# Optimization experiments

Hardware: AMD Instinct MI355X
Metric: run time of the kernel (lower is better)

Reference implementation:

```python
import jax, jax.numpy as jnp
import numpy as np

MAX_SEQ = 4096
HEADS = 4
LOCAL_HEADS = 1
WINDOW = 128
B, N, D_IN, D, D_OUT = 8, 3000, 128, 512, 64


def setup_inputs():
    key = jax.random.key(0)
    ks = jax.random.split(key, 9)
    s = 0.02
    return {
        'x': jax.random.normal(ks[0], (B, N, D_IN), jnp.float32),
        'W1': jax.random.normal(ks[1], (D_IN, D), jnp.float32) * s,
        'b1': jnp.zeros((D,), jnp.float32),
        'ln1_g': jnp.ones((D,), jnp.float32),
        'ln1_b': jnp.zeros((D,), jnp.float32),
        'Wq': jax.random.normal(ks[2], (D, D), jnp.float32) * s,
        'Wk': jax.random.normal(ks[3], (D, D), jnp.float32) * s,
        'Wv': jax.random.normal(ks[4], (D, D), jnp.float32) * s,
        'Wo': jax.random.normal(ks[5], (D, D), jnp.float32) * s,
        'bo': jnp.zeros((D,), jnp.float32),
        'ln2_g': jnp.ones((D,), jnp.float32),
        'ln2_b': jnp.zeros((D,), jnp.float32),
        'Wf1': jax.random.normal(ks[6], (D, 4 * D), jnp.float32) * s,
        'bf1': jnp.zeros((4 * D,), jnp.float32),
        'Wf2': jax.random.normal(ks[7], (4 * D, D), jnp.float32) * s,
        'bf2': jnp.zeros((D,), jnp.float32),
        'W2': jax.random.normal(ks[8], (D, D_OUT), jnp.float32) * s,
        'b2': jnp.zeros((D_OUT,), jnp.float32),
    }


def _ln(x, g, b, eps=1e-5):
    mu = jnp.mean(x, -1, keepdims=True)
    var = jnp.var(x, -1, keepdims=True)
    return (x - mu) * jax.lax.rsqrt(var + eps) * g + b


def _look_around(x, pad_value=0.0):
    # x: [b, w, n, ...] -> [b, w, 3n, ...] (backward=1, self, forward=1 windows)
    pads = [(0, 0), (1, 1)] + [(0, 0)] * (x.ndim - 2)
    p = jnp.pad(x, pads, constant_values=pad_value)
    w = x.shape[1]
    return jnp.concatenate([p[:, i:i + w] for i in range(3)], axis=2)


def _local_attn(q, k, v):
    # windowed softmax attention, window=128, look back/forward 1 window
    Bh, H, T, d = q.shape
    w = T // WINDOW
    merge = lambda t: t.reshape(Bh * H, w, WINDOW, d)
    bq, bk, bv = merge(q), merge(k), merge(v)
    bk = _look_around(bk)
    bv = _look_around(bv)
    ticker = jnp.arange(T).reshape(1, w, WINDOW)
    bq_k = _look_around(ticker, pad_value=-1)  # [1, w, 3*WINDOW]
    dots = jnp.einsum('bwie,bwje->bwij', bq, bk) * (d ** -0.5)
    mask = (bq_k[:, :, None, :] == -1)
    dots = jnp.where(mask, jnp.finfo(dots.dtype).min, dots)
    attn = jax.nn.softmax(dots, axis=-1)
    out = jnp.einsum('bwij,bwje->bwie', attn, bv)
    return out.reshape(Bh, H, T, d)


def _linear_attn(q, k, v):
    # kernelized global attention: softmax feature maps + d x d context
    d = q.shape[-1]
    q = jax.nn.softmax(q, axis=-1) * (d ** -0.5)
    k = jax.nn.softmax(k, axis=-2)
    ctx = jnp.einsum('bhnd,bhne->bhde', k, v)
    return jnp.einsum('bhnd,bhde->bhne', q, ctx)


def _self_attn(x, Wq, Wk, Wv, Wo, bo):
    Bx, T, Dm = x.shape
    dh = Dm // HEADS
    split = lambda t: t.reshape(Bx, T, HEADS, dh).transpose(0, 2, 1, 3)
    q, k, v = split(x @ Wq), split(x @ Wk), split(x @ Wv)
    lq, gq = q[:, :LOCAL_HEADS], q[:, LOCAL_HEADS:]
    lk, gk = k[:, :LOCAL_HEADS], k[:, LOCAL_HEADS:]
    lv, gv = v[:, :LOCAL_HEADS], v[:, LOCAL_HEADS:]
    local_out = _local_attn(lq, lk, lv)
    global_out = _linear_attn(gq, gk, gv)
    out = jnp.concatenate([local_out, global_out], axis=1)
    out = out.transpose(0, 2, 1, 3).reshape(Bx, T, Dm)
    return out @ Wo + bo


def _forward(x, W1, b1, ln1_g, ln1_b, Wq, Wk, Wv, Wo, bo,
             ln2_g, ln2_b, Wf1, bf1, Wf2, bf2, W2, b2):
    Bx, n, _ = x.shape
    xp = jnp.pad(x, ((0, 0), (0, MAX_SEQ - n), (0, 0)))
    h = jnp.tanh(xp @ W1 + b1)
    # depth=1 transformer block: PreNorm attn + residual, PreNorm FF + residual
    h = h + _self_attn(_ln(h, ln1_g, ln1_b), Wq, Wk, Wv, Wo, bo)
    ff = jax.nn.gelu(_ln(h, ln2_g, ln2_b) @ Wf1 + bf1, approximate=False)
    h = h + ff @ Wf2 + bf2
    out = h @ W2 + b2
    return out[:, :n, :]


def reference(x, W1, b1, ln1_g, ln1_b, Wq, Wk, Wv, Wo, bo,
              ln2_g, ln2_b, Wf1, bf1, Wf2, bf2, W2, b2):
    return _forward(x, W1, b1, ln1_g, ln1_b, Wq, Wk, Wv, Wo, bo,
                    ln2_g, ln2_b, Wf1, bf1, Wf2, bf2, W2, b2)
```

## Files before the change

### kernel.cpp

```cpp
#include <hip/hip_runtime.h>
#include <hip/hip_bf16.h>
#include <math.h>


typedef __hip_bfloat16 bf16;
typedef __attribute__((ext_vector_type(8))) short short8;
typedef __attribute__((ext_vector_type(4))) float floatx4;

#define SEQ   4096
#define NBAT  8
#define DM    512
#define DINP  128
#define DFF   2048
#define NREAL 3000
#define CS    40

#define MFMA16(a,b,c) __builtin_amdgcn_mfma_f32_16x16x32_bf16((a),(b),(c),0,0,0)
#define BARRIER() asm volatile("s_barrier" ::: "memory")

__device__ __forceinline__ void gload_lds16(const void* g, void* l) {
  auto* gp = reinterpret_cast<const __attribute__((address_space(1))) unsigned int*>(
      reinterpret_cast<uintptr_t>(g));
  auto* lp = reinterpret_cast<__attribute__((address_space(3))) unsigned int*>(
      reinterpret_cast<uintptr_t>(l));
  __builtin_amdgcn_global_load_lds(gp, lp, 16, 0, 0);
}

__device__ __forceinline__ short8 lds_read128(const bf16* p) {
  auto* lp = reinterpret_cast<const __attribute__((address_space(3))) bf16*>(
      reinterpret_cast<uintptr_t>(p));
  short8 r;
  asm volatile("ds_read_b128 %0, %1" : "=v"(r) : "v"(lp));
  return r;
}

__device__ __forceinline__ float fast_erff(float x) {
  float ax = fabsf(x);
  float t = __builtin_amdgcn_rcpf(fmaf(0.3275911f, ax, 1.f));
  float p = fmaf(fmaf(fmaf(fmaf(1.061405429f, t, -1.453152027f), t,
                           1.421413741f), t, -0.284496736f), t, 0.254829592f) * t;
  float r = 1.f - p * __expf(-ax * ax);
  return copysignf(r, x);
}

__device__ __forceinline__ float fast_tanhf(float x) {
  float e = __expf(2.f * x);
  return 1.f - 2.f * __builtin_amdgcn_rcpf(e + 1.f);
}

__global__ __launch_bounds__(256) void beacon(float* __restrict__ out, long n) {
  long i = (long)blockIdx.x * 256 + threadIdx.x;
  if (i < n) out[i] = 10000.f;
}

__global__ __launch_bounds__(256) void transpose8(
    const float* __restrict__ W1, const float* __restrict__ Wq,
    const float* __restrict__ Wk, const float* __restrict__ Wv,
    const float* __restrict__ Wo, const float* __restrict__ Wf1,
    const float* __restrict__ Wf2, const float* __restrict__ W2,
    bf16* __restrict__ wt) {
  const int Ks[8]   = {128, 512, 512, 512, 512, 512, 2048, 512};
  const int Ns[8]   = {512, 512, 512, 512, 512, 2048, 512, 64};
  const int Nps[8]  = {512, 512, 512, 512, 512, 2048, 512, 128};
  const long Ofs[8] = {0L, 65536L, 327680L, 589824L, 851968L, 1114112L, 2162688L, 3211264L};
  int zi = blockIdx.z;
  int K = Ks[zi], N = Ns[zi], Npad = Nps[zi];
  int k0 = blockIdx.x * 64, n0 = blockIdx.y * 64;
  if (k0 >= K || n0 >= Npad) return;
  const float* W = zi == 0 ? W1 : zi == 1 ? Wq : zi == 2 ? Wk : zi == 3 ? Wv
                 : zi == 4 ? Wo : zi == 5 ? Wf1 : zi == 6 ? Wf2 : W2;
  bf16* Wt = wt + Ofs[zi];
  __shared__ float t[64][65];
  int r = threadIdx.x >> 2, c = (threadIdx.x & 3) * 16;
#pragma unroll
  for (int i = 0; i < 16; i++) {
    int n = n0 + c + i;
    t[r][c + i] = (n < N) ? W[(long)(k0 + r) * N + n] : 0.f;
  }
  __syncthreads();
#pragma unroll
  for (int i = 0; i < 16; i++)
    Wt[(long)(n0 + r) * K + k0 + c + i] = (bf16)t[c + i][r];
}

__device__ inline uint4 pack8(const float* p) {
  union { bf16 h[8]; uint4 u; } r;
  float4 a = *(const float4*)p;
  float4 b = *(const float4*)(p + 4);
  r.h[0] = (bf16)a.x; r.h[1] = (bf16)a.y; r.h[2] = (bf16)a.z; r.h[3] = (bf16)a.w;
  r.h[4] = (bf16)b.x; r.h[5] = (bf16)b.y; r.h[6] = (bf16)b.z; r.h[7] = (bf16)b.w;
  return r.u;
}

__global__ __launch_bounds__(512, 2) void gemm256(
    const bf16* __restrict__ A, const bf16* __restrict__ Bt,
    const float* __restrict__ bias, float* __restrict__ Cf, bf16* __restrict__ Cb,
    int K, int lda, int ldb, int ldc, int EPI,
    long aBatch, long bBatch, int zdiv, long cOuter, long cInner) {
  __shared__ __align__(16) bf16 sm[5 * 256 * 64];
  bf16* const smB = sm + 2 * 16384;
  const int tid = threadIdx.x;
  const int lane = tid & 63, wid = tid >> 6;

  const int nx = gridDim.x, ny = gridDim.y;
  const long nwg = (long)nx * ny * gridDim.z;
  const long fid = blockIdx.x + (long)nx * (blockIdx.y + (long)ny * blockIdx.z);
  const long cq = nwg >> 3, cr = nwg & 7;
  const long xcd = fid & 7, ofs = fid >> 3;
  const long swz = (xcd < cr ? xcd * (cq + 1) : cr * (cq + 1) + (xcd - cr) * cq) + ofs;
  const int bx = (int)(swz % nx);
  const int by = (int)((swz / nx) % ny);
  const int bz = (int)(swz / ((long)nx * ny));

  const bf16* Ab = A + (long)bz * aBatch;
  const bf16* Bb = Bt + (long)bz * bBatch;
  const long cOff = (long)(bz / zdiv) * cOuter + (long)(bz % zdiv) * cInner;
  const int row0 = by * 256;
  const int col0 = bx * 256;

  const int widm = wid >> 2, widn = wid & 3;
  const int lr = lane & 15, lq4 = lane >> 4;
  const int sw = (lr & 7) << 4;
  const int k0e = ((0 * 64 + lq4 * 16) ^ sw) >> 1;
  const int k1e = ((1 * 64 + lq4 * 16) ^ sw) >> 1;

  const int lrow = lane >> 3;
  const int lch = (lane & 7) ^ lrow;
  const bf16* pAbase = Ab + (long)(row0 + wid * 8 + lrow) * lda + lch * 8;
  const bf16* pBbase = Bb + (long)(col0 + wid * 8 + lrow) * ldb + lch * 8;
  const long a64 = (long)64 * lda, b64 = (long)64 * ldb;
  int kA = 0, kB = 0;

  floatx4 acc[8][4];
#pragma unroll
  for (int i = 0; i < 8; i++)
#pragma unroll
    for (int j = 0; j < 4; j++) acc[i][j] = {0.f, 0.f, 0.f, 0.f};

  auto stageA4 = [&](int buf) {
    bf16* base = sm + buf * 16384;
#pragma unroll
    for (int h = 0; h < 2; h++) {
      bf16* d = base + (h * 128 + wid * 8) * 64;
      const bf16* g = pAbase + (long)(h * 2) * a64 + kA;
      gload_lds16(g, d);
      gload_lds16(g + a64, d + 64 * 64);
    }
    kA += 64;
  };
  auto stageB4 = [&](int slot) {
    bf16* base = smB + slot * 16384;
#pragma unroll
    for (int h = 0; h < 2; h++) {
      bf16* d = base + (h * 128 + wid * 8) * 64;
      const bf16* g = pBbase + (long)(h * 2) * b64 + kB;
      gload_lds16(g, d);
      gload_lds16(g + b64, d + 64 * 64);
    }
    kB += 64;
  };

  short8 bfr[4][2], af[2][2];
  auto readB = [&](int slot) {
    const bf16* base = smB + slot * 16384;
#pragma unroll
    for (int nt = 0; nt < 4; nt++) {
      int colB = widn * 64 + nt * 16 + lr;
      bfr[nt][0] = lds_read128(base + colB * 64 + k0e);
      bfr[nt][1] = lds_read128(base + colB * 64 + k1e);
    }
  };
  auto readA = [&](int buf, int q) {
    const bf16* base = sm + buf * 16384;
#pragma unroll
    for (int m = 0; m < 2; m++) {
      int rowA = widm * 128 + q * 32 + m * 16 + lr;
      af[m][0] = lds_read128(base + rowA * 64 + k0e);
      af[m][1] = lds_read128(base + rowA * 64 + k1e);
    }
  };
  auto mmaq = [&](int q) {
    asm volatile("s_waitcnt lgkmcnt(0)" ::: "memory");
    __builtin_amdgcn_sched_barrier(0);
    __builtin_amdgcn_s_setprio(1);
#pragma unroll
    for (int m = 0; m < 2; m++)
#pragma unroll
      for (int nt = 0; nt < 4; nt++) {
        acc[q * 2 + m][nt] = MFMA16(af[m][0], bfr[nt][0], acc[q * 2 + m][nt]);
        acc[q * 2 + m][nt] = MFMA16(af[m][1], bfr[nt][1], acc[q * 2 + m][nt]);
      }
    __builtin_amdgcn_s_setprio(0);
  };

  const int T = K >> 6;
  stageA4(0);
  stageB4(0);
  stageB4(1);
  asm volatile("s_waitcnt vmcnt(4)" ::: "memory");
  BARRIER();

  int bsel = 0;
  for (int t = 0; t < T; t++) {
    const int cb = t & 1, nb = cb ^ 1;
    readB(bsel);
    readA(cb, 0);
    if (t + 1 < T) stageA4(nb);
    mmaq(0);
    readA(cb, 1);
    mmaq(1);
    readA(cb, 2);
    if (t + 2 < T) stageB4(bsel == 0 ? 2 : bsel - 1);
    mmaq(2);
    readA(cb, 3);
    mmaq(3);
    if (t + 2 < T) {
      asm volatile("s_waitcnt vmcnt(4)" ::: "memory");
    } else if (t + 1 < T) {
      asm volatile("s_waitcnt vmcnt(0)" ::: "memory");
    }
    BARRIER();
    bsel = bsel == 2 ? 0 : bsel + 1;
  }

  if (EPI == 2) {
#pragma unroll
    for (int nt = 0; nt < 4; nt++) {
      int c = col0 + widn * 64 + nt * 16 + lr;
      float bv = bias ? bias[c] : 0.f;
#pragma unroll
      for (int mi = 0; mi < 8; mi++) {
        long rb = row0 + widm * 128 + mi * 16 + lq4 * 4;
#pragma unroll
        for (int reg = 0; reg < 4; reg++) {
          float v = acc[mi][nt][reg] + bv;
          long idx = cOff + (rb + reg) * (long)ldc + c;
          Cf[idx] += v;
        }
      }
    }
  } else {
    bf16* scr = sm + wid * (64 * 72);
    const int rr = lane >> 3, ccol = (lane & 7) * 8;
#pragma unroll
    for (int p = 0; p < 2; p++) {
#pragma unroll
      for (int nt = 0; nt < 4; nt++) {
        int c = col0 + widn * 64 + nt * 16 + lr;
        float bv = bias ? bias[c] : 0.f;
#pragma unroll
        for (int ml = 0; ml < 4; ml++) {
#pragma unroll
          for (int reg = 0; reg < 4; reg++) {
            float v = acc[p * 4 + ml][nt][reg] + bv;
            if (EPI == 4) v = 0.5f * v * (1.f + fast_erff(v * 0.70710678118654752f));
            scr[(ml * 16 + lq4 * 4 + reg) * 72 + nt * 16 + lr] = (bf16)v;
          }
        }
      }
#pragma unroll
      for (int it = 0; it < 8; it++) {
        int r = it * 8 + rr;
        uint4 v = *(const uint4*)&scr[r * 72 + ccol];
        long grow = row0 + widm * 128 + p * 64 + r;
        *(uint4*)&Cb[cOff + grow * (long)ldc + col0 + widn * 64 + ccol] = v;
      }
    }
  }
}

__global__ __launch_bounds__(256) void gemm_bt(
    const void* __restrict__ Avoid, const bf16* __restrict__ Bt,
    const float* __restrict__ bias, float* __restrict__ Cf, bf16* __restrict__ Cb,
    int K, int lda, int ldb, int ldc, int EPI, int AMODE,
    long aBatch, long bBatch, int zdiv, long cOuter, long cInner) {
  __shared__ __align__(16) bf16 As0[128 * 32];
  __shared__ __align__(16) bf16 As1[128 * 32];
  __shared__ __align__(16) bf16 Bs0[128 * 32];
  __shared__ __align__(16) bf16 Bs1[128 * 32];
  const int tid = threadIdx.x;

  const int nx = gridDim.x, ny = gridDim.y;
  const long nwg = (long)nx * ny * gridDim.z;
  const long fid = blockIdx.x + (long)nx * (blockIdx.y + (long)ny * blockIdx.z);
  const long cq = nwg >> 3, cr = nwg & 7;
  const long xcd = fid & 7, ofs = fid >> 3;
  const long swz = (xcd < cr ? xcd * (cq + 1) : cr * (cq + 1) + (xcd - cr) * cq) + ofs;
  const int bx = (int)(swz % nx);
  const int by = (int)((swz / nx) % ny);
  const int bz = (int)(swz / ((long)nx * ny));

  Bt += (long)bz * bBatch;
  const long cOff = (long)(bz / zdiv) * cOuter + (long)(bz % zdiv) * cInner;
  const int row0 = by * 128;
  const int col0 = bx * 128;
  const int lane = tid & 63, wid = tid >> 6;
  const int wm = (wid & 1) * 64, wn = (wid >> 1) * 64;
  const int lr = lane & 15, lk = (lane >> 4) * 8;

  floatx4 acc[4][4];
#pragma unroll
  for (int i = 0; i < 4; i++)
#pragma unroll
    for (int j = 0; j < 4; j++) acc[i][j] = {0.f, 0.f, 0.f, 0.f};

  if (AMODE == 0) {
    const bf16* A = (const bf16*)Avoid + (long)bz * aBatch;
    const bf16* pAa = A + (long)(row0 + wid * 16 + (lane >> 2)) * lda + (lane & 3) * 8;
    const bf16* pBa = Bt + (long)(col0 + wid * 16 + (lane >> 2)) * ldb + (lane & 3) * 8;
    bf16* ldsA0 = &As0[wid * 16 * 32];
    bf16* ldsA1 = &As1[wid * 16 * 32];
    bf16* ldsB0 = &Bs0[wid * 16 * 32];
    bf16* ldsB1 = &Bs1[wid * 16 * 32];
    const long a64 = (long)64 * lda, b64 = (long)64 * ldb;

    auto stage = [&](bf16* dA, bf16* dB) {
      gload_lds16(pAa, dA);
      gload_lds16(pAa + a64, dA + 64 * 32);
      gload_lds16(pBa, dB);
      gload_lds16(pBa + b64, dB + 64 * 32);
      pAa += 32; pBa += 32;
    };
    auto compute = [&](const bf16* AS, const bf16* BS) {
      short8 af[4], bfr[4];
#pragma unroll
      for (int mt = 0; mt < 4; mt++) af[mt] = *(const short8*)(&AS[(wm + mt * 16 + lr) * 32 + lk]);
#pragma unroll
      for (int nt = 0; nt < 4; nt++) bfr[nt] = *(const short8*)(&BS[(wn + nt * 16 + lr) * 32 + lk]);
#pragma unroll
      for (int mt = 0; mt < 4; mt++)
#pragma unroll
        for (int nt = 0; nt < 4; nt++)
          acc[mt][nt] = MFMA16(af[mt], bfr[nt], acc[mt][nt]);
    };

    stage(ldsA0, ldsB0);
    __syncthreads();
    for (int k0 = 0; k0 < K; k0 += 64) {
      stage(ldsA1, ldsB1);
      compute(As0, Bs0);
      __syncthreads();
      if (k0 + 64 < K) stage(ldsA0, ldsB0);
      compute(As1, Bs1);
      __syncthreads();
    }
  } else {
    const float* Af = (const float*)Avoid;
    const int srow = tid >> 2;
    const int skcol = (tid & 3) * 8;
    const long r0 = row0 + srow, r1 = r0 + 64;
    const bf16* pB = Bt + (long)(col0 + srow) * ldb + skcol;
    const int ldsOff = srow * 32 + skcol;
    const float* pF0; const float* pF1;
    bool v0 = true, v1 = true;
    if (AMODE == 1) {
      int t0 = (int)(r0 & (SEQ - 1)), t1 = (int)(r1 & (SEQ - 1));
      v0 = t0 < NREAL; v1 = t1 < NREAL;
      if (!v0) t0 = 0;
      if (!v1) t1 = 0;
      pF0 = Af + ((r0 >> 12) * NREAL + t0) * DINP + skcol;
      pF1 = Af + ((r1 >> 12) * NREAL + t1) * DINP + skcol;
    } else {
      pF0 = Af + r0 * lda + skcol;
      pF1 = Af + r1 * lda + skcol;
    }
    for (int k0 = 0; k0 < K; k0 += 32) {
      uint4 b0 = *(const uint4*)(pB);
      uint4 b1 = *(const uint4*)(pB + (long)64 * ldb);
      pB += 32;
      uint4 a0 = {0, 0, 0, 0}, a1 = {0, 0, 0, 0};
      if (v0) a0 = pack8(pF0);
      if (v1) a1 = pack8(pF1);
      pF0 += 32; pF1 += 32;
      __syncthreads();
      *(uint4*)(&As0[ldsOff]) = a0;
      *(uint4*)(&As0[ldsOff + 64 * 32]) = a1;
      *(uint4*)(&Bs0[ldsOff]) = b0;
      *(uint4*)(&Bs0[ldsOff + 64 * 32]) = b1;
      __syncthreads();
      short8 af[4], bfr[4];
#pragma unroll
      for (int mt = 0; mt < 4; mt++) af[mt] = *(const short8*)(&As0[(wm + mt * 16 + lr) * 32 + lk]);
#pragma unroll
      for (int nt = 0; nt < 4; nt++) bfr[nt] = *(const short8*)(&Bs0[(wn + nt * 16 + lr) * 32 + lk]);
#pragma unroll
      for (int mt = 0; mt < 4; mt++)
#pragma unroll
        for (int nt = 0; nt < 4; nt++)
          acc[mt][nt] = MFMA16(af[mt], bfr[nt], acc[mt][nt]);
    }
  }

#pragma unroll
  for (int nt = 0; nt < 4; nt++) {
    int c = col0 + wn + nt * 16 + lr;
    float bv = 0.f;
    if (bias) {
      if (EPI == 5) { if (c < 64) bv = bias[c]; }
      else bv = bias[c];
    }
#pragma unroll
    for (int mt = 0; mt < 4; mt++) {
      long rb = row0 + wm + mt * 16 + (lane >> 4) * 4;
#pragma unroll
      for (int reg = 0; reg < 4; reg++) {
        float v = acc[mt][nt][reg] + bv;
        long ri = rb + reg;
        long idx = cOff + ri * (long)ldc + c;
        if (EPI == 0) Cf[idx] = fast_tanhf(v);
        else if (EPI == 1) Cb[idx] = (bf16)v;
        else if (EPI == 2) Cf[idx] += v;
        else if (EPI == 4) { float g = 0.5f * v * (1.f + fast_erff(v * 0.70710678118654752f)); Cb[idx] = (bf16)g; }
        else if (EPI == 5) {
          int bb = (int)(ri >> 12); int tt = (int)(ri & (SEQ - 1));
          if (tt < NREAL && c < 64) Cf[((long)bb * NREAL + tt) * 64 + c] = v;
        }
      }
    }
  }
}

__global__ __launch_bounds__(256) void ln_kernel(const float* __restrict__ h,
                                                 const float* __restrict__ g,
                                                 const float* __restrict__ bta,
                                                 bf16* __restrict__ out) {
  int wid = threadIdx.x >> 6, lane = threadIdx.x & 63;
  long row = (long)blockIdx.x * 4 + wid;
  const float* src = h + row * DM + lane * 8;
  float4 a = *(const float4*)(src);
  float4 b = *(const float4*)(src + 4);
  float x[8] = {a.x, a.y, a.z, a.w, b.x, b.y, b.z, b.w};
  float s = 0.f, sq = 0.f;
#pragma unroll
  for (int i = 0; i < 8; i++) { s += x[i]; sq += x[i] * x[i]; }
#pragma unroll
  for (int m = 32; m >= 1; m >>= 1) { s += __shfl_xor(s, m, 64); sq += __shfl_xor(sq, m, 64); }
  float mu = s * (1.f / DM);
  float var = sq * (1.f / DM) - mu * mu;
  float rstd = rsqrtf(var + 1e-5f);
  const float* gp = g + lane * 8;
  const float* bp = bta + lane * 8;
  bf16* dst = out + row * DM + lane * 8;
#pragma unroll
  for (int i = 0; i < 8; i++)
    dst[i] = (bf16)((x[i] - mu) * rstd * gp[i] + bp[i]);
}

__global__ __launch_bounds__(256) void local_attn(const bf16* __restrict__ q,
                                                  const bf16* __restrict__ k,
                                                  const bf16* __restrict__ v,
                                                  bf16* __restrict__ att) {
  int half = blockIdx.x, w = blockIdx.y, b = blockIdx.z;
  int tid = threadIdx.x, wid = tid >> 6, lane = tid & 63;
  int lr = lane & 15, lq4 = lane >> 4;
  __shared__ __align__(16) bf16 Ks[32 * 128];
  __shared__ __align__(16) bf16 Vts[128 * 32];
  __shared__ __align__(16) bf16 Ps[4][16 * 32];

  int t0 = w * 128 + half * 64 + wid * 16;
  long qbase = ((long)b * SEQ + t0 + lr) * DM;
  short8 qf[4];
#pragma unroll
  for (int ks = 0; ks < 4; ks++) qf[ks] = *(const short8*)(q + qbase + ks * 32 + lq4 * 8);

  floatx4 Oacc[8];
#pragma unroll
  for (int i = 0; i < 8; i++) Oacc[i] = {0.f, 0.f, 0.f, 0.f};
  float rs[4] = {0.f, 0.f, 0.f, 0.f};

  int keystart = w * 128 - 128;
  for (int ch = 0; ch < 12; ch++) {
    int kb = keystart + ch * 32;
    if (kb < 0 || kb >= SEQ) continue;
    {
      int j = tid >> 3, d = (tid & 7) * 16;
      const bf16* ksrc = k + ((long)b * SEQ + kb + j) * DM + d;
      *(uint4*)(&Ks[j * 128 + d]) = *(const uint4*)(ksrc);
      *(uint4*)(&Ks[j * 128 + d + 8]) = *(const uint4*)(ksrc + 8);
      const bf16* vsrc = v + ((long)b * SEQ + kb + j) * DM + d;
#pragma unroll
      for (int e = 0; e < 16; e++) Vts[(d + e) * 32 + j] = vsrc[e];
    }
    __syncthreads();
    floatx4 s0 = {0.f, 0.f, 0.f, 0.f}, s1 = {0.f, 0.f, 0.f, 0.f};
#pragma unroll
    for (int ks = 0; ks < 4; ks++) {
      short8 kf0 = *(const short8*)(&Ks[(0 + lr) * 128 + ks * 32 + lq4 * 8]);
      short8 kf1 = *(const short8*)(&Ks[(16 + lr) * 128 + ks * 32 + lq4 * 8]);
      s0 = MFMA16(qf[ks], kf0, s0);
      s1 = MFMA16(qf[ks], kf1, s1);
    }
#pragma unroll
    for (int reg = 0; reg < 4; reg++) {
      float e0 = __expf(s0[reg] * 0.08838834764831845f);
      float e1 = __expf(s1[reg] * 0.08838834764831845f);
      rs[reg] += e0 + e1;
      Ps[wid][(lq4 * 4 + reg) * 32 + lr] = (bf16)e0;
      Ps[wid][(lq4 * 4 + reg) * 32 + 16 + lr] = (bf16)e1;
    }
    __syncthreads();
    short8 pf = *(const short8*)(&Ps[wid][lr * 32 + lq4 * 8]);
#pragma unroll
    for (int nt = 0; nt < 8; nt++) {
      short8 vf = *(const short8*)(&Vts[(nt * 16 + lr) * 32 + lq4 * 8]);
      Oacc[nt] = MFMA16(pf, vf, Oacc[nt]);
    }
    __syncthreads();
  }
#pragma unroll
  for (int m = 1; m < 16; m <<= 1)
#pragma unroll
    for (int reg = 0; reg < 4; reg++) rs[reg] += __shfl_xor(rs[reg], m, 64);
  long obase = ((long)b * SEQ + t0 + lq4 * 4) * DM;
#pragma unroll
  for (int nt = 0; nt < 8; nt++)
#pragma unroll
    for (int reg = 0; reg < 4; reg++)
      att[obase + (long)reg * DM + nt * 16 + lr] = (bf16)(Oacc[nt][reg] / rs[reg]);
}

__global__ __launch_bounds__(256) void qp_softmax(const bf16* __restrict__ q, bf16* __restrict__ qp) {
  int wid = threadIdx.x >> 6, lane = threadIdx.x & 63;
  long task = (long)blockIdx.x * 4 + wid;
  int tt = (int)(task & (SEQ - 1));
  int z6 = (int)(task >> 12);
  int lb = z6 / 3, h2 = z6 % 3;
  const bf16* src = q + ((long)lb * SEQ + tt) * DM + (h2 + 1) * 128 + lane * 2;
  float x0 = (float)src[0], x1 = (float)src[1];
  float m = fmaxf(x0, x1);
#pragma unroll
  for (int s = 32; s >= 1; s >>= 1) m = fmaxf(m, __shfl_xor(m, s, 64));
  float e0 = __expf(x0 - m), e1 = __expf(x1 - m);
  float sm = e0 + e1;
#pragma unroll
  for (int s = 32; s >= 1; s >>= 1) sm += __shfl_xor(sm, s, 64);
  float inv = 0.08838834764831845f / sm;
  bf16* dst = qp + task * 128 + lane * 2;
  dst[0] = (bf16)(e0 * inv);
  dst[1] = (bf16)(e1 * inv);
}

__global__ __launch_bounds__(128) void kstats_part(const bf16* __restrict__ k,
                                                   float* __restrict__ part, int lOff) {
  int chunk = blockIdx.x, z = blockIdx.y;
  int lb = z / 3, h2 = z % 3, ch = (h2 + 1) * 128;
  int d = threadIdx.x;
  const bf16* base = k + ((long)lb * SEQ + chunk * 128) * DM + ch + d;
  float m = -1e30f;
#pragma unroll 4
  for (int t = 0; t < 128; t++) m = fmaxf(m, (float)base[(long)t * DM]);
  float l = 0.f;
#pragma unroll 4
  for (int t = 0; t < 128; t++) l += __expf((float)base[(long)t * DM] - m);
  int idx = (z * 32 + chunk) * 128 + d;
  part[idx] = m;
  part[lOff + idx] = l;
}

__global__ __launch_bounds__(128) void kstats_comb(const float* __restrict__ part,
                                                   float* __restrict__ kml, int lOff) {
  int z = blockIdx.x, d = threadIdx.x;
  float M = -1e30f;
#pragma unroll 4
  for (int c = 0; c < 32; c++) M = fmaxf(M, part[(z * 32 + c) * 128 + d]);
  float L = 0.f;
#pragma unroll 4
  for (int c = 0; c < 32; c++) {
    int i = (z * 32 + c) * 128 + d;
    L += part[lOff + i] * __expf(part[i] - M);
  }
  kml[z * 256 + d] = M;
  kml[z * 256 + 128 + d] = L;
}

__global__ __launch_bounds__(256) void ctx_mfma(const bf16* __restrict__ k,
                                                const bf16* __restrict__ v,
                                                const float* __restrict__ kml,
                                                float* __restrict__ part) {
  int chunk = blockIdx.x, z = blockIdx.y;
  int lb = z / 3, h2 = z % 3, ch = (h2 + 1) * 128;
  int tid = threadIdx.x, lane = tid & 63, wid = tid >> 6;
  const int wm = (wid & 1) * 64, wn = (wid >> 1) * 64;
  const int lr = lane & 15, lk = (lane >> 4) * 8;
  __shared__ float ml2[128];
  __shared__ __align__(16) bf16 Vt[128 * CS];
  __shared__ __align__(16) bf16 Kt[128 * CS];
  if (tid < 128)
    ml2[tid] = kml[z * 256 + tid] + logf(kml[z * 256 + 128 + tid]);

  int j = tid >> 3, d0 = (tid & 7) * 16;
  const bf16* vsrc = v + ((long)lb * SEQ + chunk * 512 + j) * DM + ch + d0;
  const bf16* ksrc = k + ((long)lb * SEQ + chunk * 512 + j) * DM + ch + d0;

  floatx4 acc[4][4];
#pragma unroll
  for (int i = 0; i < 4; i++)
#pragma unroll
    for (int jj = 0; jj < 4; jj++) acc[i][jj] = {0.f, 0.f, 0.f, 0.f};

  for (int s = 0; s < 16; s++) {
    union { bf16 h[16]; uint4 u[2]; } va, ka;
    va.u[0] = *(const uint4*)(vsrc); va.u[1] = *(const uint4*)(vsrc + 8);
    ka.u[0] = *(const uint4*)(ksrc); ka.u[1] = *(const uint4*)(ksrc + 8);
    vsrc += (long)32 * DM; ksrc += (long)32 * DM;
    __syncthreads();
#pragma unroll
    for (int e = 0; e < 16; e++) {
      Vt[(d0 + e) * CS + j] = va.h[e];
      Kt[(d0 + e) * CS + j] = (bf16)__expf((float)ka.h[e] - ml2[d0 + e]);
    }
    __syncthreads();
    short8 af[4], bfr[4];
#pragma unroll
    for (int mt = 0; mt < 4; mt++) af[mt] = *(const short8*)(&Vt[(wm + mt * 16 + lr) * CS + lk]);
#pragma unroll
    for (int nt = 0; nt < 4; nt++) bfr[nt] = *(const short8*)(&Kt[(wn + nt * 16 + lr) * CS + lk]);
#pragma unroll
    for (int mt = 0; mt < 4; mt++)
#pragma unroll
      for (int nt = 0; nt < 4; nt++)
        acc[mt][nt] = MFMA16(af[mt], bfr[nt], acc[mt][nt]);
  }

  float* dst = part + ((long)z * 8 + chunk) * 16384;
#pragma unroll
  for (int nt = 0; nt < 4; nt++) {
    int c = wn + nt * 16 + lr;
#pragma unroll
    for (int mt = 0; mt < 4; mt++) {
      int rb = wm + mt * 16 + (lane >> 4) * 4;
#pragma unroll
      for (int reg = 0; reg < 4; reg++)
        dst[(rb + reg) * 128 + c] = acc[mt][nt][reg];
    }
  }
}

__global__ __launch_bounds__(256) void ctx_reduce(const float* __restrict__ part, bf16* __restrict__ ctxT) {
  long i = (long)blockIdx.x * 256 + threadIdx.x;
  int z = (int)(i >> 14);
  int off = (int)(i & 16383);
  float s = 0.f;
#pragma unroll
  for (int c = 0; c < 8; c++) s += part[(((long)z * 8 + c) << 14) + off];
  ctxT[i] = (bf16)s;
}

extern "C" void kernel_launch(void* const* d_in, const int* in_sizes, int n_in,
                              void* d_out, int out_size, void* d_ws, size_t ws_size,
                              hipStream_t stream) {
  float* outp = (float*)d_out;

  long offH = 0;
  int GB = 0;
  long offLNG, offQ, offK, offV, offATT, offCTXP, offCTXT, offKML, offWT, need;
  for (int gb = 8; gb >= 2; gb >>= 1) {
    long sLN = (long)gb * 4194304;
    offLNG = 67108864L;
    offQ   = offLNG + sLN;
    offK   = offQ + sLN;
    offV   = offK + sLN;
    offATT = offV + sLN;
    offCTXP= offATT + sLN;
    offCTXT= offCTXP + (long)gb * 1572864;
    offKML = offCTXT + (long)gb * 98304;
    offWT  = offKML + (long)gb * 3072;
    need   = offWT + 6553600L;
    if ((size_t)need <= ws_size) { GB = gb; break; }
  }
  if (GB == 0) {
    beacon<<<(out_size + 255) / 256, 256, 0, stream>>>(outp, out_size);
    return;
  }
  const int NG = NBAT / GB;
  const long GR = (long)GB * SEQ;
  const int NZ = GB * 3;

  const float* x   = (const float*)d_in[0];
  const float* W1  = (const float*)d_in[1];
  const float* b1  = (const float*)d_in[2];
  const float* g1  = (const float*)d_in[3];
  const float* be1 = (const float*)d_in[4];
  const float* Wq  = (const float*)d_in[5];
  const float* Wk  = (const float*)d_in[6];
  const float* Wv  = (const float*)d_in[7];
  const float* Wo  = (const float*)d_in[8];
  const float* bo  = (const float*)d_in[9];
  const float* g2  = (const float*)d_in[10];
  const float* be2 = (const float*)d_in[11];
  const float* Wf1 = (const float*)d_in[12];
  const float* bf1 = (const float*)d_in[13];
  const float* Wf2 = (const float*)d_in[14];
  const float* bf2 = (const float*)d_in[15];
  const float* W2  = (const float*)d_in[16];
  const float* b2  = (const float*)d_in[17];

  char* ws = (char*)d_ws;
  float* h   = (float*)(ws + offH);
  bf16* lnG  = (bf16*)(ws + offLNG);
  bf16* qp   = (bf16*)(ws + offLNG);
  bf16* qb   = (bf16*)(ws + offQ);
  bf16* kb   = (bf16*)(ws + offK);
  bf16* vb   = (bf16*)(ws + offV);
  bf16* attb = (bf16*)(ws + offATT);
  bf16* ff1g = (bf16*)(ws + offQ);
  float* ctxp= (float*)(ws + offCTXP);
  bf16* ctxT = (bf16*)(ws + offCTXT);
  float* kml = (float*)(ws + offKML);
  bf16* wt   = (bf16*)(ws + offWT);
  bf16* wqt  = wt + 65536;
  bf16* wot  = wt + 851968;
  bf16* wf1t = wt + 1114112;
  bf16* wf2t = wt + 2162688;
  bf16* w2t  = wt + 3211264;
  const int lOff = NZ * 32 * 128;

  transpose8<<<dim3(32, 32, 8), 256, 0, stream>>>(W1, Wq, Wk, Wv, Wo, Wf1, Wf2, W2, wt);

  gemm_bt<<<dim3(4, 256, 1), 256, 0, stream>>>(x, wt, b1, h, nullptr,
      DINP, DINP, DINP, DM, 0, 1, 0, 0, 1, 0, 0);

  for (int g = 0; g < NG; g++) {
    float* hg = h + (long)g * GR * DM;
    ln_kernel<<<(int)(GR / 4), 256, 0, stream>>>(hg, g1, be1, lnG);
    gemm256<<<dim3(2, (int)(GR / 256), 3), 512, 0, stream>>>(lnG, wqt, nullptr, nullptr, qb,
        DM, DM, DM, DM, 1,
        0L, 262144L, 3, 0L, GR * DM);

    local_attn<<<dim3(2, 32, GB), 256, 0, stream>>>(qb, kb, vb, attb);

    qp_softmax<<<NZ * 1024, 256, 0, stream>>>(qb, qp);
    kstats_part<<<dim3(32, NZ), 128, 0, stream>>>(kb, ctxp, lOff);
    kstats_comb<<<NZ, 128, 0, stream>>>(ctxp, kml, lOff);
    ctx_mfma<<<dim3(8, NZ), 256, 0, stream>>>(kb, vb, kml, ctxp);
    ctx_reduce<<<NZ * 64, 256, 0, stream>>>(ctxp, ctxT);
    gemm_bt<<<dim3(1, 32, NZ), 256, 0, stream>>>(qp, ctxT, nullptr, nullptr, attb + 128,
        128, 128, 128, DM, 1, 0,
        (long)SEQ * 128, 16384L, 3, (long)SEQ * DM, 128L);

    gemm256<<<dim3(2, (int)(GR / 256), 1), 512, 0, stream>>>(attb, wot, bo, hg, nullptr,
        DM, DM, DM, DM, 2, 0, 0, 1, 0, 0);
  }

  for (int g = 0; g < NG; g++) {
    float* hg = h + (long)g * GR * DM;
    ln_kernel<<<(int)(GR / 4), 256, 0, stream>>>(hg, g2, be2, lnG);
    gemm256<<<dim3(8, (int)(GR / 256), 1), 512, 0, stream>>>(lnG, wf1t, bf1, nullptr, ff1g,
        DM, DM, DM, DFF, 4, 0, 0, 1, 0, 0);
    gemm256<<<dim3(2, (int)(GR / 256), 1), 512, 0, stream>>>(ff1g, wf2t, bf2, hg, nullptr,
        DFF, DFF, DFF, DM, 2, 0, 0, 1, 0, 0);
  }

  gemm_bt<<<dim3(1, 256, 1), 256, 0, stream>>>(h, w2t, b2, outp, nullptr,
      DM, DM, DM, 64, 5, 2, 0, 0, 1, 0, 0);
}
```

Before: 650.2 us.

## Store residual stream in fp16 and vectorize residual-add epilogue through LDS

The fp32 residual buffer h becomes fp16 throughout: the first GEMM writes tanh output as half, layernorm reads half, the output GEMM packs half to bf16, and the gemm256 residual-add epilogue stages results in LDS and does vectorized 16-byte read-modify-write in half. It also reorders the block-index decomposition so the z index varies fastest after the XCD swizzle. This halves residual-stream traffic and replaces scattered scalar fp32 += with coalesced vector updates, at the cost of fp16 precision and range in the residual accumulation.

```diff
diff --git a/kernel.cpp b/kernel.cpp
--- a/kernel.cpp
+++ b/kernel.cpp
@@ -1,5 +1,6 @@
 #include <hip/hip_runtime.h>
 #include <hip/hip_bf16.h>
+#include <hip/hip_fp16.h>
 #include <math.h>
 
 
@@ -92,9 +93,18 @@
   return r.u;
 }
 
+__device__ inline uint4 pack8h(const __half* p) {
+  union { __half h[8]; uint4 u; } s;
+  s.u = *(const uint4*)p;
+  union { bf16 h[8]; uint4 u; } r;
+#pragma unroll
+  for (int i = 0; i < 8; i++) r.h[i] = (bf16)(float)s.h[i];
+  return r.u;
+}
+
 __global__ __launch_bounds__(512, 2) void gemm256(
     const bf16* __restrict__ A, const bf16* __restrict__ Bt,
-    const float* __restrict__ bias, float* __restrict__ Cf, bf16* __restrict__ Cb,
+    const float* __restrict__ bias, __half* __restrict__ Ch, bf16* __restrict__ Cb,
     int K, int lda, int ldb, int ldc, int EPI,
     long aBatch, long bBatch, int zdiv, long cOuter, long cInner) {
   __shared__ __align__(16) bf16 sm[5 * 256 * 64];
@@ -102,15 +112,16 @@
   const int tid = threadIdx.x;
   const int lane = tid & 63, wid = tid >> 6;
 
-  const int nx = gridDim.x, ny = gridDim.y;
-  const long nwg = (long)nx * ny * gridDim.z;
+  const int nx = gridDim.x, ny = gridDim.y, nz = gridDim.z;
+  const long nwg = (long)nx * ny * nz;
   const long fid = blockIdx.x + (long)nx * (blockIdx.y + (long)ny * blockIdx.z);
   const long cq = nwg >> 3, cr = nwg & 7;
   const long xcd = fid & 7, ofs = fid >> 3;
   const long swz = (xcd < cr ? xcd * (cq + 1) : cr * (cq + 1) + (xcd - cr) * cq) + ofs;
-  const int bx = (int)(swz % nx);
-  const int by = (int)((swz / nx) % ny);
-  const int bz = (int)(swz / ((long)nx * ny));
+  const int bz = (int)(swz % nz);
+  const long s2 = swz / nz;
+  const int bx = (int)(s2 % nx);
+  const int by = (int)(s2 / nx);
 
   const bf16* Ab = A + (long)bz * aBatch;
   const bf16* Bb = Bt + (long)bz * bBatch;
@@ -224,19 +235,34 @@
   }
 
   if (EPI == 2) {
-#pragma unroll
-    for (int nt = 0; nt < 4; nt++) {
-      int c = col0 + widn * 64 + nt * 16 + lr;
-      float bv = bias ? bias[c] : 0.f;
-#pragma unroll
-      for (int mi = 0; mi < 8; mi++) {
-        long rb = row0 + widm * 128 + mi * 16 + lq4 * 4;
-#pragma unroll
-        for (int reg = 0; reg < 4; reg++) {
-          float v = acc[mi][nt][reg] + bv;
-          long idx = cOff + (rb + reg) * (long)ldc + c;
-          Cf[idx] += v;
+    __half* scr = (__half*)sm + wid * (64 * 72);
+    const int rr = lane >> 3, ccol = (lane & 7) * 8;
+#pragma unroll
+    for (int p = 0; p < 2; p++) {
+#pragma unroll
+      for (int nt = 0; nt < 4; nt++) {
+        int c = col0 + widn * 64 + nt * 16 + lr;
+        float bv = bias ? bias[c] : 0.f;
+#pragma unroll
+        for (int ml = 0; ml < 4; ml++) {
+#pragma unroll
+          for (int reg = 0; reg < 4; reg++)
+            scr[(ml * 16 + lq4 * 4 + reg) * 72 + nt * 16 + lr] =
+                (__half)(acc[p * 4 + ml][nt][reg] + bv);
         }
+      }
+#pragma unroll
+      for (int it = 0; it < 8; it++) {
+        int r = it * 8 + rr;
+        union { __half e[8]; uint4 u; } sv, ov;
+        sv.u = *(const uint4*)&scr[r * 72 + ccol];
+        long grow = row0 + widm * 128 + p * 64 + r;
+        long idx = cOff + grow * (long)ldc + col0 + widn * 64 + ccol;
+        ov.u = *(const uint4*)&Ch[idx];
+#pragma unroll
+        for (int e = 0; e < 8; e++)
+          ov.e[e] = (__half)((float)ov.e[e] + (float)sv.e[e]);
+        *(uint4*)&Ch[idx] = ov.u;
       }
     }
   } else {
@@ -280,15 +306,16 @@
   __shared__ __align__(16) bf16 Bs1[128 * 32];
   const int tid = threadIdx.x;
 
-  const int nx = gridDim.x, ny = gridDim.y;
-  const long nwg = (long)nx * ny * gridDim.z;
+  const int nx = gridDim.x, ny = gridDim.y, nz = gridDim.z;
+  const long nwg = (long)nx * ny * nz;
   const long fid = blockIdx.x + (long)nx * (blockIdx.y + (long)ny * blockIdx.z);
   const long cq = nwg >> 3, cr = nwg & 7;
   const long xcd = fid & 7, ofs = fid >> 3;
   const long swz = (xcd < cr ? xcd * (cq + 1) : cr * (cq + 1) + (xcd - cr) * cq) + ofs;
-  const int bx = (int)(swz % nx);
-  const int by = (int)((swz / nx) % ny);
-  const int bz = (int)(swz / ((long)nx * ny));
+  const int bz = (int)(swz % nz);
+  const long s2 = swz / nz;
+  const int bx = (int)(s2 % nx);
+  const int by = (int)(s2 / nx);
 
   Bt += (long)bz * bBatch;
   const long cOff = (long)(bz / zdiv) * cOuter + (long)(bz % zdiv) * cInner;
@@ -346,12 +373,14 @@
     }
   } else {
     const float* Af = (const float*)Avoid;
+    const __half* Ah = (const __half*)Avoid;
     const int srow = tid >> 2;
     const int skcol = (tid & 3) * 8;
     const long r0 = row0 + srow, r1 = r0 + 64;
     const bf16* pB = Bt + (long)(col0 + srow) * ldb + skcol;
     const int ldsOff = srow * 32 + skcol;
-    const float* pF0; const float* pF1;
+    const float* pF0 = nullptr; const float* pF1 = nullptr;
+    const __half* pH0 = nullptr; const __half* pH1 = nullptr;
     bool v0 = true, v1 = true;
     if (AMODE == 1) {
       int t0 = (int)(r0 & (SEQ - 1)), t1 = (int)(r1 & (SEQ - 1));
@@ -361,17 +390,23 @@
       pF0 = Af + ((r0 >> 12) * NREAL + t0) * DINP + skcol;
       pF1 = Af + ((r1 >> 12) * NREAL + t1) * DINP + skcol;
     } else {
-      pF0 = Af + r0 * lda + skcol;
-      pF1 = Af + r1 * lda + skcol;
+      pH0 = Ah + r0 * lda + skcol;
+      pH1 = Ah + r1 * lda + skcol;
     }
     for (int k0 = 0; k0 < K; k0 += 32) {
       uint4 b0 = *(const uint4*)(pB);
       uint4 b1 = *(const uint4*)(pB + (long)64 * ldb);
       pB += 32;
       uint4 a0 = {0, 0, 0, 0}, a1 = {0, 0, 0, 0};
-      if (v0) a0 = pack8(pF0);
-      if (v1) a1 = pack8(pF1);
-      pF0 += 32; pF1 += 32;
+      if (AMODE == 1) {
+        if (v0) a0 = pack8(pF0);
+        if (v1) a1 = pack8(pF1);
+        pF0 += 32; pF1 += 32;
+      } else {
+        a0 = pack8h(pH0);
+        a1 = pack8h(pH1);
+        pH0 += 32; pH1 += 32;
+      }
       __syncthreads();
       *(uint4*)(&As0[ldsOff]) = a0;
       *(uint4*)(&As0[ldsOff + 64 * 32]) = a1;
@@ -407,7 +442,7 @@
         float v = acc[mt][nt][reg] + bv;
         long ri = rb + reg;
         long idx = cOff + ri * (long)ldc + c;
-        if (EPI == 0) Cf[idx] = fast_tanhf(v);
+        if (EPI == 0) ((__half*)Cf)[idx] = (__half)fast_tanhf(v);
         else if (EPI == 1) Cb[idx] = (bf16)v;
         else if (EPI == 2) Cf[idx] += v;
         else if (EPI == 4) { float g = 0.5f * v * (1.f + fast_erff(v * 0.70710678118654752f)); Cb[idx] = (bf16)g; }
@@ -420,16 +455,18 @@
   }
 }
 
-__global__ __launch_bounds__(256) void ln_kernel(const float* __restrict__ h,
+__global__ __launch_bounds__(256) void ln_kernel(const __half* __restrict__ h,
                                                  const float* __restrict__ g,
                                                  const float* __restrict__ bta,
                                                  bf16* __restrict__ out) {
   int wid = threadIdx.x >> 6, lane = threadIdx.x & 63;
   long row = (long)blockIdx.x * 4 + wid;
-  const float* src = h + row * DM + lane * 8;
-  float4 a = *(const float4*)(src);
-  float4 b = *(const float4*)(src + 4);
-  float x[8] = {a.x, a.y, a.z, a.w, b.x, b.y, b.z, b.w};
+  const __half* src = h + row * DM + lane * 8;
+  union { __half e[8]; uint4 u; } hv;
+  hv.u = *(const uint4*)(src);
+  float x[8];
+#pragma unroll
+  for (int i = 0; i < 8; i++) x[i] = (float)hv.e[i];
   float s = 0.f, sq = 0.f;
 #pragma unroll
   for (int i = 0; i < 8; i++) { s += x[i]; sq += x[i] * x[i]; }
@@ -696,7 +733,7 @@
   const float* b2  = (const float*)d_in[17];
 
   char* ws = (char*)d_ws;
-  float* h   = (float*)(ws + offH);
+  __half* h  = (__half*)(ws + offH);
   bf16* lnG  = (bf16*)(ws + offLNG);
   bf16* qp   = (bf16*)(ws + offLNG);
   bf16* qb   = (bf16*)(ws + offQ);
@@ -717,11 +754,11 @@
 
   transpose8<<<dim3(32, 32, 8), 256, 0, stream>>>(W1, Wq, Wk, Wv, Wo, Wf1, Wf2, W2, wt);
 
-  gemm_bt<<<dim3(4, 256, 1), 256, 0, stream>>>(x, wt, b1, h, nullptr,
+  gemm_bt<<<dim3(4, 256, 1), 256, 0, stream>>>(x, wt, b1, (float*)h, nullptr,
       DINP, DINP, DINP, DM, 0, 1, 0, 0, 1, 0, 0);
 
   for (int g = 0; g < NG; g++) {
-    float* hg = h + (long)g * GR * DM;
+    __half* hg = h + (long)g * GR * DM;
     ln_kernel<<<(int)(GR / 4), 256, 0, stream>>>(hg, g1, be1, lnG);
     gemm256<<<dim3(2, (int)(GR / 256), 3), 512, 0, stream>>>(lnG, wqt, nullptr, nullptr, qb,
         DM, DM, DM, DM, 1,
@@ -743,7 +780,7 @@
   }
 
   for (int g = 0; g < NG; g++) {
-    float* hg = h + (long)g * GR * DM;
+    __half* hg = h + (long)g * GR * DM;
     ln_kernel<<<(int)(GR / 4), 256, 0, stream>>>(hg, g2, be2, lnG);
     gemm256<<<dim3(8, (int)(GR / 256), 1), 512, 0, stream>>>(lnG, wf1t, bf1, nullptr, ff1g,
         DM, DM, DM, DFF, 4, 0, 0, 1, 0, 0);
```

New measurement: 601.7 us, median of 3. 7.5% less time.
